# Kernel tuning notes

Hardware: AMD Instinct MI355X
Metric: run time of the kernel (lower is better)

The kernel has to match this reference:

```python
import jax, jax.numpy as jnp
import numpy as np


def setup_inputs() -> dict:
    key = jax.random.key(0)
    k1, k2, k3, k4, k5 = jax.random.split(key, 5)
    N, E, C_in, C_out = 100000, 1600000, 64, 64
    x = jax.random.normal(k1, (N, C_in), dtype=jnp.float32)
    edge_index = jax.random.randint(k2, (2, E), 0, N, dtype=jnp.int64)
    edge_weight = jax.random.uniform(k3, (E,), dtype=jnp.float32)
    # Xavier-uniform Linear weights [out, in], zero biases (matches reset_parameters)
    bound = float(np.sqrt(6.0 / (C_in + C_out)))
    W_self = jax.random.uniform(k4, (C_out, C_in), dtype=jnp.float32, minval=-bound, maxval=bound)
    W_neigh = jax.random.uniform(k5, (C_out, C_in), dtype=jnp.float32, minval=-bound, maxval=bound)
    b_self = jnp.zeros((C_out,), dtype=jnp.float32)
    b_neigh = jnp.zeros((C_out,), dtype=jnp.float32)
    return {"x": x, "edge_index": edge_index, "edge_weight": edge_weight,
            "W_self": W_self, "b_self": b_self, "W_neigh": W_neigh, "b_neigh": b_neigh,
            "num_nodes": N}


def reference(x, edge_index, edge_weight, W_self, b_self, W_neigh, b_neigh, num_nodes):
    row, col = edge_index[0], edge_index[1]
    # gather source features, weight, scatter-add to destinations: [E, C] -> [N, C]
    message = x[col] * edge_weight[:, None]
    neigh_agg = jax.ops.segment_sum(message, row, num_segments=num_nodes)
    # two linear projections (torch Linear: y = x @ W.T + b)
    return x @ W_self.T + b_self + neigh_agg @ W_neigh.T + b_neigh
```

## Files before the change

### kernel.cpp

```cpp
#include <hip/hip_runtime.h>
#include <hip/hip_bf16.h>


#define C 64
#define BKT 128
#define MAXB 800
#define BINT 6144
#define BTHR 1024
#define CAP 2560

typedef __attribute__((ext_vector_type(8))) short bf16x8;
typedef __attribute__((ext_vector_type(4))) float f32x4;

__device__ inline unsigned short f2bf(float f) {
    union { __hip_bfloat16 h; unsigned short u; } c;
    c.h = __float2bfloat16(f);
    return c.u;
}

__device__ inline float bfhi(unsigned short u) {
    return __int_as_float(((int)u) << 16);
}

__global__ __launch_bounds__(256) void prep_kernel(
        const int* __restrict__ ei, int* __restrict__ bhist, int E, int NBK,
        const float* __restrict__ x, unsigned short* __restrict__ xb, int n4) {
    __shared__ int lh[MAXB];
    const int t = threadIdx.x;
    for (int i = t; i < NBK; i += 256) lh[i] = 0;
    __syncthreads();
    const int gtid = blockIdx.x * 256 + t;
    const int gs = gridDim.x * 256;
    for (int e = gtid; e < E; e += gs)
        atomicAdd(&lh[ei[e] >> 7], 1);
    __syncthreads();
    for (int i = t; i < NBK; i += 256)
        if (lh[i]) atomicAdd(&bhist[i], lh[i]);
    const float4* x4 = (const float4*)x;
    ushort4* xb4 = (ushort4*)xb;
    for (int i = gtid; i < n4; i += gs) {
        float4 v = x4[i];
        ushort4 o;
        o.x = f2bf(v.x); o.y = f2bf(v.y); o.z = f2bf(v.z); o.w = f2bf(v.w);
        xb4[i] = o;
    }
}

__global__ __launch_bounds__(1024) void scan_kernel(
        const int* __restrict__ bhist, int* __restrict__ boffs,
        int* __restrict__ bcur, int NBK) {
    __shared__ int s[1024];
    const int t = threadIdx.x;
    s[t] = (t < NBK) ? bhist[t] : 0;
    __syncthreads();
    for (int off = 1; off < 1024; off <<= 1) {
        int v = 0;
        if (t >= off) v = s[t - off];
        __syncthreads();
        if (t >= off) s[t] += v;
        __syncthreads();
    }
    if (t < NBK) {
        int e = (t > 0) ? s[t - 1] : 0;
        boffs[t] = e;
        bcur[t] = e;
        if (t == NBK - 1) boffs[NBK] = s[t];
    }
}

__global__ __launch_bounds__(BTHR) void bin_kernel(
        const int* __restrict__ ei, const float* __restrict__ ew,
        int* __restrict__ bcur, const int* __restrict__ unused,
        int2* __restrict__ sorted, int E, int NBK) {
    __shared__ int2 stage[BINT];
    __shared__ unsigned short stageb[BINT];
    __shared__ int h[MAXB];
    __shared__ int cur[MAXB];
    __shared__ int adj[MAXB];
    __shared__ int wsum[16];

    const int t = threadIdx.x;
    const int lane = t & 63;
    const int wv = t >> 6;
    const int e0 = blockIdx.x * BINT;
    const int cnt = min(BINT, E - e0);

    for (int i = t; i < NBK; i += BTHR) h[i] = 0;
    __syncthreads();

#pragma unroll
    for (int k = 0; k < BINT / BTHR; ++k) {
        const int idx = t + k * BTHR;
        if (idx < cnt) atomicAdd(&h[ei[e0 + idx] >> 7], 1);
    }
    __syncthreads();

    const int val = (t < NBK) ? h[t] : 0;
    int v = val;
#pragma unroll
    for (int off = 1; off < 64; off <<= 1) {
        const int u = __shfl_up(v, off);
        if (lane >= off) v += u;
    }
    if (lane == 63) wsum[wv] = v;
    __syncthreads();
    if (t < 64) {
        int s = (lane < 16) ? wsum[lane] : 0;
#pragma unroll
        for (int off = 1; off < 16; off <<= 1) {
            const int u = __shfl_up(s, off);
            if (lane >= off) s += u;
        }
        if (lane < 16) wsum[lane] = s;
    }
    __syncthreads();
    if (t < NBK) {
        const int incl = v + ((wv > 0) ? wsum[wv - 1] : 0);
        const int excl = incl - val;
        cur[t] = excl;
        const int g = val ? atomicAdd(&bcur[t], val) : 0;
        adj[t] = g - excl;
    }
    __syncthreads();

#pragma unroll
    for (int k = 0; k < BINT / BTHR; ++k) {
        const int idx = t + k * BTHR;
        if (idx < cnt) {
            const int e = e0 + idx;
            const int d = ei[e];
            const int s = ei[E + e];
            const float w = ew[e];
            const int b = d >> 7;
            const int dl = d & 127;
            const int p = atomicAdd(&cur[b], 1);
            stage[p] = make_int2((dl << 17) | s, __float_as_int(w));
            stageb[p] = (unsigned short)b;
        }
    }
    __syncthreads();

    for (int i = t; i < cnt; i += BTHR) {
        const int b = stageb[i];
        sorted[adj[b] + i] = stage[i];
    }
}

__global__ __launch_bounds__(512) void agg_kernel(
        const ushort4* __restrict__ xb4,
        const int2* __restrict__ sorted,
        const int* __restrict__ boffs,
        float* __restrict__ agg, int N) {
    __shared__ int2 meta2[CAP];
    __shared__ int lcnt[BKT];
    __shared__ int lincl[BKT];
    __shared__ int lcur[BKT];

    const int t = threadIdx.x;
    const int b = blockIdx.x;
    const int node0 = b << 7;
    const int lane = t & 63;
    const int wv = t >> 6;
    const int q = lane >> 4;
    const int cq = lane & 15;

    const int beg = boffs[b];
    const int end = boffs[b + 1];

    int chunk = beg;
    do {
        const int cc = (end - chunk < CAP) ? (end - chunk) : CAP;

        for (int i = t; i < BKT; i += 512) lcnt[i] = 0;
        __syncthreads();

        for (int i = t; i < cc; i += 512)
            atomicAdd(&lcnt[sorted[chunk + i].x >> 17], 1);
        __syncthreads();

        if (t < BKT) lincl[t] = lcnt[t];
        __syncthreads();
        for (int off = 1; off < BKT; off <<= 1) {
            int v = 0;
            if (t < BKT && t >= off) v = lincl[t - off];
            __syncthreads();
            if (t < BKT && t >= off) lincl[t] += v;
            __syncthreads();
        }
        if (t < BKT) lcur[t] = lincl[t] - lcnt[t];
        __syncthreads();

        for (int i = t; i < cc; i += 512) {
            const int2 m = sorted[chunk + i];
            const int dl = m.x >> 17;
            const int p = atomicAdd(&lcur[dl], 1);
            meta2[p] = make_int2(m.x & 0x1FFFF, m.y);
        }
        __syncthreads();

        const bool first = (chunk == beg);
        for (int r = wv; r < BKT; r += 8) {
            const int s1 = lincl[r];
            const int s0 = s1 - lcnt[r];
            float a0 = 0.f, a1 = 0.f, a2 = 0.f, a3 = 0.f;
            int j = s0 + q;
            for (; j + 4 < s1; j += 8) {
                const int2 m0 = meta2[j];
                const int2 m1 = meta2[j + 4];
                const ushort4 u0 = xb4[(unsigned)m0.x * 16u + cq];
                const ushort4 u1 = xb4[(unsigned)m1.x * 16u + cq];
                const float w0 = __int_as_float(m0.y);
                const float w1 = __int_as_float(m1.y);
                a0 += w0 * bfhi(u0.x); a1 += w0 * bfhi(u0.y);
                a2 += w0 * bfhi(u0.z); a3 += w0 * bfhi(u0.w);
                a0 += w1 * bfhi(u1.x); a1 += w1 * bfhi(u1.y);
                a2 += w1 * bfhi(u1.z); a3 += w1 * bfhi(u1.w);
            }
            if (j < s1) {
                const int2 m0 = meta2[j];
                const ushort4 u0 = xb4[(unsigned)m0.x * 16u + cq];
                const float w0 = __int_as_float(m0.y);
                a0 += w0 * bfhi(u0.x); a1 += w0 * bfhi(u0.y);
                a2 += w0 * bfhi(u0.z); a3 += w0 * bfhi(u0.w);
            }
            a0 += __shfl_xor(a0, 16); a0 += __shfl_xor(a0, 32);
            a1 += __shfl_xor(a1, 16); a1 += __shfl_xor(a1, 32);
            a2 += __shfl_xor(a2, 16); a2 += __shfl_xor(a2, 32);
            a3 += __shfl_xor(a3, 16); a3 += __shfl_xor(a3, 32);
            const int node = node0 + r;
            if (q == 0 && node < N) {
                float4* dst = (float4*)(agg + (size_t)node * C + 4 * cq);
                if (first) {
                    *dst = make_float4(a0, a1, a2, a3);
                } else {
                    float4 o = *dst;
                    o.x += a0; o.y += a1; o.z += a2; o.w += a3;
                    *dst = o;
                }
            }
        }
        chunk += CAP;
        __syncthreads();
    } while (chunk < end);
}

__global__ __launch_bounds__(256) void scatter_kernel(
        const float* __restrict__ x, const int* __restrict__ ei,
        const float* __restrict__ ew, float* __restrict__ agg, int E) {
    const int lane = threadIdx.x & 63;
    const int wid = (blockIdx.x * blockDim.x + threadIdx.x) >> 6;
    const int nw = (gridDim.x * blockDim.x) >> 6;
    for (int base = wid * 64; base < E; base += nw * 64) {
        const int e = base + lane;
        int dst = 0, src = 0; float w = 0.f;
        if (e < E) { dst = ei[e]; src = ei[E + e]; w = ew[e]; }
        const int cnt = min(64, E - base);
        for (int j = 0; j < cnt; ++j) {
            const int d = __shfl(dst, j);
            const int s = __shfl(src, j);
            const float wj = __shfl(w, j);
            atomicAdd(&agg[d * C + lane], x[s * C + lane] * wj);
        }
    }
}

__device__ inline bf16x8 cvt8(const float* __restrict__ p) {
    f32x4 lo = *(const f32x4*)p;
    f32x4 hi = *(const f32x4*)(p + 4);
    union { bf16x8 v; __hip_bfloat16 e[8]; } u;
#pragma unroll
    for (int j = 0; j < 4; ++j) u.e[j] = __float2bfloat16(lo[j]);
#pragma unroll
    for (int j = 0; j < 4; ++j) u.e[4 + j] = __float2bfloat16(hi[j]);
    return u.v;
}

__global__ __launch_bounds__(256) void proj_kernel(
        const float* __restrict__ x, const float* __restrict__ agg,
        const float* __restrict__ Ws, const float* __restrict__ bs,
        const float* __restrict__ Wn, const float* __restrict__ bn,
        float* __restrict__ out, int N) {
    const int lane = threadIdx.x & 63;
    const int wid = (blockIdx.x * blockDim.x + threadIdx.x) >> 6;
    const int l15 = lane & 15;
    const int quad = lane >> 4;
    const int nTiles = N >> 4;
    if (wid >= nTiles) return;
    const int m0 = wid << 4;

    bf16x8 bsf[4][2], bnf[4][2];
#pragma unroll
    for (int tt = 0; tt < 4; ++tt) {
        const int o = tt * 16 + l15;
#pragma unroll
        for (int h = 0; h < 2; ++h) {
            bsf[tt][h] = cvt8(Ws + o * C + h * 32 + quad * 8);
            bnf[tt][h] = cvt8(Wn + o * C + h * 32 + quad * 8);
        }
    }

    const int m = m0 + l15;
    bf16x8 ax[2], ag[2];
#pragma unroll
    for (int h = 0; h < 2; ++h) {
        ax[h] = cvt8(x + m * C + h * 32 + quad * 8);
        ag[h] = cvt8(agg + m * C + h * 32 + quad * 8);
    }

#pragma unroll
    for (int tt = 0; tt < 4; ++tt) {
        f32x4 acc = {0.f, 0.f, 0.f, 0.f};
        acc = __builtin_amdgcn_mfma_f32_16x16x32_bf16(ax[0], bsf[tt][0], acc, 0, 0, 0);
        acc = __builtin_amdgcn_mfma_f32_16x16x32_bf16(ax[1], bsf[tt][1], acc, 0, 0, 0);
        acc = __builtin_amdgcn_mfma_f32_16x16x32_bf16(ag[0], bnf[tt][0], acc, 0, 0, 0);
        acc = __builtin_amdgcn_mfma_f32_16x16x32_bf16(ag[1], bnf[tt][1], acc, 0, 0, 0);
        const int o = tt * 16 + l15;
        const float bias = bs[o] + bn[o];
#pragma unroll
        for (int r = 0; r < 4; ++r)
            out[(m0 + quad * 4 + r) * C + o] = acc[r] + bias;
    }
}

extern "C" void kernel_launch(void* const* d_in, const int* in_sizes, int n_in,
                              void* d_out, int out_size, void* d_ws, size_t ws_size,
                              hipStream_t stream) {
    const float* x  = (const float*)d_in[0];
    const int*   ei = (const int*)d_in[1];
    const float* ew = (const float*)d_in[2];
    const float* Ws = (const float*)d_in[3];
    const float* bs = (const float*)d_in[4];
    const float* Wn = (const float*)d_in[5];
    const float* bn = (const float*)d_in[6];

    const int N = in_sizes[0] / C;
    const int E = in_sizes[2];
    const int NBK = (N + BKT - 1) / BKT;

    char* p = (char*)d_ws;
    float* agg = (float*)p;                 p += (size_t)N * C * sizeof(float);
    unsigned short* xb = (unsigned short*)p; p += (size_t)N * C * sizeof(short);
    int2* sorted = (int2*)p;                p += (size_t)E * sizeof(int2);
    int* bhist = (int*)p;                   p += (size_t)MAXB * sizeof(int);
    int* boffs = (int*)p;                   p += (size_t)(MAXB + 1) * sizeof(int);
    int* bcur = (int*)p;                    p += (size_t)MAXB * sizeof(int);
    const size_t needed = (size_t)(p - (char*)d_ws);

    const int nTiles = N / 16;
    const int projBlocks = (nTiles + 3) / 4;

    if (needed <= ws_size && N <= (1 << 17) && NBK <= MAXB) {
        const int n4 = N * C / 4;
        hipMemsetAsync(bhist, 0, (size_t)NBK * sizeof(int), stream);
        prep_kernel<<<1024, 256, 0, stream>>>(ei, bhist, E, NBK, x, xb, n4);
        scan_kernel<<<1, 1024, 0, stream>>>(bhist, boffs, bcur, NBK);
        bin_kernel<<<(E + BINT - 1) / BINT, BTHR, 0, stream>>>(ei, ew, bcur, bhist,
                                                               sorted, E, NBK);
        agg_kernel<<<NBK, 512, 0, stream>>>((const ushort4*)xb, sorted,
                                            boffs, agg, N);
    } else {
        hipMemsetAsync(agg, 0, (size_t)N * C * sizeof(float), stream);
        scatter_kernel<<<2048, 256, 0, stream>>>(x, ei, ew, agg, E);
    }

    proj_kernel<<<projBlocks, 256, 0, stream>>>(x, agg, Ws, bs, Wn, bn,
                                                (float*)d_out, N);
}
```

Baseline: 215.4 us.

## Widen agg gathers to 16B, write bf16 aggregate, add bf16-input projection

The aggregation kernel now loads 8 bf16 channels per lane with 16-byte loads, using 8 edge groups per wave instead of 4. It reduces the results with a transposing shuffle tree so every lane stores one channel. On the final chunk it writes the aggregate directly as bf16. A new projection kernel reads the bf16 x, the bf16 aggregate and the pre-converted bf16 weights, so the fp32 reads and in-kernel conversions disappear from the projection. The aim is fewer gather transactions and less projection traffic, at the cost of an extra bf16 buffer and more shuffle work.

```diff
diff --git a/kernel.cpp b/kernel.cpp
--- a/kernel.cpp
+++ b/kernel.cpp
@@ -18,13 +18,18 @@
     return c.u;
 }
 
-__device__ inline float bfhi(unsigned short u) {
-    return __int_as_float(((int)u) << 16);
+__device__ inline float bflo16(unsigned int u) {
+    return __int_as_float((int)(u << 16));
+}
+__device__ inline float bfhi16(unsigned int u) {
+    return __int_as_float((int)(u & 0xFFFF0000u));
 }
 
 __global__ __launch_bounds__(256) void prep_kernel(
         const int* __restrict__ ei, int* __restrict__ bhist, int E, int NBK,
-        const float* __restrict__ x, unsigned short* __restrict__ xb, int n4) {
+        const float* __restrict__ x, unsigned short* __restrict__ xb, int n4,
+        const float* __restrict__ Ws, const float* __restrict__ Wn,
+        unsigned short* __restrict__ Wsb, unsigned short* __restrict__ Wnb) {
     __shared__ int lh[MAXB];
     const int t = threadIdx.x;
     for (int i = t; i < NBK; i += 256) lh[i] = 0;
@@ -43,6 +48,15 @@
         ushort4 o;
         o.x = f2bf(v.x); o.y = f2bf(v.y); o.z = f2bf(v.z); o.w = f2bf(v.w);
         xb4[i] = o;
+    }
+    if (gtid < 1024) {
+        float4 v = ((const float4*)Ws)[gtid];
+        ushort4 o;
+        o.x = f2bf(v.x); o.y = f2bf(v.y); o.z = f2bf(v.z); o.w = f2bf(v.w);
+        ((ushort4*)Wsb)[gtid] = o;
+        v = ((const float4*)Wn)[gtid];
+        o.x = f2bf(v.x); o.y = f2bf(v.y); o.z = f2bf(v.z); o.w = f2bf(v.w);
+        ((ushort4*)Wnb)[gtid] = o;
     }
 }
 
@@ -147,10 +161,12 @@
 }
 
 __global__ __launch_bounds__(512) void agg_kernel(
-        const ushort4* __restrict__ xb4,
+        const unsigned short* __restrict__ xb,
         const int2* __restrict__ sorted,
         const int* __restrict__ boffs,
-        float* __restrict__ agg, int N) {
+        float* __restrict__ agg,
+        unsigned short* __restrict__ aggb,
+        int N) {
     __shared__ int2 meta2[CAP];
     __shared__ int lcnt[BKT];
     __shared__ int lincl[BKT];
@@ -161,8 +177,15 @@
     const int node0 = b << 7;
     const int lane = t & 63;
     const int wv = t >> 6;
-    const int q = lane >> 4;
-    const int cq = lane & 15;
+    const int oct = lane >> 3;
+    const int co = lane & 7;
+
+    const bool h1 = (lane & 8) != 0;
+    const bool h2 = (lane & 16) != 0;
+    const bool h3 = (lane & 32) != 0;
+    const int ch = co * 8 + (h1 ? 4 : 0) + (h2 ? 2 : 0) + (h3 ? 1 : 0);
+
+    const uint4* xb8 = (const uint4*)xb;
 
     const int beg = boffs[b];
     const int end = boffs[b + 1];
@@ -199,43 +222,63 @@
         __syncthreads();
 
         const bool first = (chunk == beg);
+        const bool last = (chunk + CAP >= end);
+
         for (int r = wv; r < BKT; r += 8) {
             const int s1 = lincl[r];
             const int s0 = s1 - lcnt[r];
             float a0 = 0.f, a1 = 0.f, a2 = 0.f, a3 = 0.f;
-            int j = s0 + q;
-            for (; j + 4 < s1; j += 8) {
+            float a4 = 0.f, a5 = 0.f, a6 = 0.f, a7 = 0.f;
+            int j = s0 + oct;
+            for (; j + 8 < s1; j += 16) {
                 const int2 m0 = meta2[j];
-                const int2 m1 = meta2[j + 4];
-                const ushort4 u0 = xb4[(unsigned)m0.x * 16u + cq];
-                const ushort4 u1 = xb4[(unsigned)m1.x * 16u + cq];
+                const int2 m1 = meta2[j + 8];
+                const uint4 u0 = xb8[(unsigned)m0.x * 8u + co];
+                const uint4 u1 = xb8[(unsigned)m1.x * 8u + co];
                 const float w0 = __int_as_float(m0.y);
                 const float w1 = __int_as_float(m1.y);
-                a0 += w0 * bfhi(u0.x); a1 += w0 * bfhi(u0.y);
-                a2 += w0 * bfhi(u0.z); a3 += w0 * bfhi(u0.w);
-                a0 += w1 * bfhi(u1.x); a1 += w1 * bfhi(u1.y);
-                a2 += w1 * bfhi(u1.z); a3 += w1 * bfhi(u1.w);
+                a0 += w0 * bflo16(u0.x); a1 += w0 * bfhi16(u0.x);
+                a2 += w0 * bflo16(u0.y); a3 += w0 * bfhi16(u0.y);
+                a4 += w0 * bflo16(u0.z); a5 += w0 * bfhi16(u0.z);
+                a6 += w0 * bflo16(u0.w); a7 += w0 * bfhi16(u0.w);
+                a0 += w1 * bflo16(u1.x); a1 += w1 * bfhi16(u1.x);
+                a2 += w1 * bflo16(u1.y); a3 += w1 * bfhi16(u1.y);
+                a4 += w1 * bflo16(u1.z); a5 += w1 * bfhi16(u1.z);
+                a6 += w1 * bflo16(u1.w); a7 += w1 * bfhi16(u1.w);
             }
             if (j < s1) {
                 const int2 m0 = meta2[j];
-                const ushort4 u0 = xb4[(unsigned)m0.x * 16u + cq];
+                const uint4 u0 = xb8[(unsigned)m0.x * 8u + co];
                 const float w0 = __int_as_float(m0.y);
-                a0 += w0 * bfhi(u0.x); a1 += w0 * bfhi(u0.y);
-                a2 += w0 * bfhi(u0.z); a3 += w0 * bfhi(u0.w);
+                a0 += w0 * bflo16(u0.x); a1 += w0 * bfhi16(u0.x);
+                a2 += w0 * bflo16(u0.y); a3 += w0 * bfhi16(u0.y);
+                a4 += w0 * bflo16(u0.z); a5 += w0 * bfhi16(u0.z);
+                a6 += w0 * bflo16(u0.w); a7 += w0 * bfhi16(u0.w);
             }
-            a0 += __shfl_xor(a0, 16); a0 += __shfl_xor(a0, 32);
-            a1 += __shfl_xor(a1, 16); a1 += __shfl_xor(a1, 32);
-            a2 += __shfl_xor(a2, 16); a2 += __shfl_xor(a2, 32);
-            a3 += __shfl_xor(a3, 16); a3 += __shfl_xor(a3, 32);
+            float r0 = __shfl_xor(h1 ? a0 : a4, 8);
+            float r1 = __shfl_xor(h1 ? a1 : a5, 8);
+            float r2 = __shfl_xor(h1 ? a2 : a6, 8);
+            float r3 = __shfl_xor(h1 ? a3 : a7, 8);
+            const float b0 = (h1 ? a4 : a0) + r0;
+            const float b1 = (h1 ? a5 : a1) + r1;
+            const float b2 = (h1 ? a6 : a2) + r2;
+            const float b3 = (h1 ? a7 : a3) + r3;
+            float r4 = __shfl_xor(h2 ? b0 : b2, 16);
+            float r5 = __shfl_xor(h2 ? b1 : b3, 16);
+            const float c0 = (h2 ? b2 : b0) + r4;
+            const float c1 = (h2 ? b3 : b1) + r5;
+            float r6 = __shfl_xor(h3 ? c0 : c1, 32);
+            float vfin = (h3 ? c1 : c0) + r6;
+
             const int node = node0 + r;
-            if (q == 0 && node < N) {
-                float4* dst = (float4*)(agg + (size_t)node * C + 4 * cq);
-                if (first) {
-                    *dst = make_float4(a0, a1, a2, a3);
+            if (node < N) {
+                const size_t off = (size_t)node * C + ch;
+                if (last) {
+                    if (!first) vfin += agg[off];
+                    aggb[off] = f2bf(vfin);
                 } else {
-                    float4 o = *dst;
-                    o.x += a0; o.y += a1; o.z += a2; o.w += a3;
-                    *dst = o;
+                    if (first) agg[off] = vfin;
+                    else       agg[off] += vfin;
                 }
             }
         }
@@ -322,6 +365,54 @@
     }
 }
 
+__global__ __launch_bounds__(256) void projb_kernel(
+        const unsigned short* __restrict__ xb,
+        const unsigned short* __restrict__ aggb,
+        const unsigned short* __restrict__ Wsb, const float* __restrict__ bs,
+        const unsigned short* __restrict__ Wnb, const float* __restrict__ bn,
+        float* __restrict__ out, int N) {
+    const int lane = threadIdx.x & 63;
+    const int wid = (blockIdx.x * blockDim.x + threadIdx.x) >> 6;
+    const int l15 = lane & 15;
+    const int quad = lane >> 4;
+    const int nTiles = N >> 4;
+    if (wid >= nTiles) return;
+    const int m0 = wid << 4;
+
+    bf16x8 bsf[4][2], bnf[4][2];
+#pragma unroll
+    for (int tt = 0; tt < 4; ++tt) {
+        const int o = tt * 16 + l15;
+#pragma unroll
+        for (int h = 0; h < 2; ++h) {
+            bsf[tt][h] = *(const bf16x8*)(Wsb + o * C + h * 32 + quad * 8);
+            bnf[tt][h] = *(const bf16x8*)(Wnb + o * C + h * 32 + quad * 8);
+        }
+    }
+
+    const int m = m0 + l15;
+    bf16x8 ax[2], ag[2];
+#pragma unroll
+    for (int h = 0; h < 2; ++h) {
+        ax[h] = *(const bf16x8*)(xb + (size_t)m * C + h * 32 + quad * 8);
+        ag[h] = *(const bf16x8*)(aggb + (size_t)m * C + h * 32 + quad * 8);
+    }
+
+#pragma unroll
+    for (int tt = 0; tt < 4; ++tt) {
+        f32x4 acc = {0.f, 0.f, 0.f, 0.f};
+        acc = __builtin_amdgcn_mfma_f32_16x16x32_bf16(ax[0], bsf[tt][0], acc, 0, 0, 0);
+        acc = __builtin_amdgcn_mfma_f32_16x16x32_bf16(ax[1], bsf[tt][1], acc, 0, 0, 0);
+        acc = __builtin_amdgcn_mfma_f32_16x16x32_bf16(ag[0], bnf[tt][0], acc, 0, 0, 0);
+        acc = __builtin_amdgcn_mfma_f32_16x16x32_bf16(ag[1], bnf[tt][1], acc, 0, 0, 0);
+        const int o = tt * 16 + l15;
+        const float bias = bs[o] + bn[o];
+#pragma unroll
+        for (int r = 0; r < 4; ++r)
+            out[(m0 + quad * 4 + r) * C + o] = acc[r] + bias;
+    }
+}
+
 extern "C" void kernel_launch(void* const* d_in, const int* in_sizes, int n_in,
                               void* d_out, int out_size, void* d_ws, size_t ws_size,
                               hipStream_t stream) {
@@ -338,12 +429,15 @@
     const int NBK = (N + BKT - 1) / BKT;
 
     char* p = (char*)d_ws;
-    float* agg = (float*)p;                 p += (size_t)N * C * sizeof(float);
-    unsigned short* xb = (unsigned short*)p; p += (size_t)N * C * sizeof(short);
-    int2* sorted = (int2*)p;                p += (size_t)E * sizeof(int2);
-    int* bhist = (int*)p;                   p += (size_t)MAXB * sizeof(int);
-    int* boffs = (int*)p;                   p += (size_t)(MAXB + 1) * sizeof(int);
-    int* bcur = (int*)p;                    p += (size_t)MAXB * sizeof(int);
+    float* agg = (float*)p;                  p += (size_t)N * C * sizeof(float);
+    unsigned short* xb = (unsigned short*)p;  p += (size_t)N * C * sizeof(short);
+    unsigned short* aggb = (unsigned short*)p; p += (size_t)N * C * sizeof(short);
+    int2* sorted = (int2*)p;                 p += (size_t)E * sizeof(int2);
+    unsigned short* Wsb = (unsigned short*)p; p += (size_t)C * C * sizeof(short);
+    unsigned short* Wnb = (unsigned short*)p; p += (size_t)C * C * sizeof(short);
+    int* bhist = (int*)p;                    p += (size_t)MAXB * sizeof(int);
+    int* boffs = (int*)p;                    p += (size_t)(MAXB + 1) * sizeof(int);
+    int* bcur = (int*)p;                     p += (size_t)MAXB * sizeof(int);
     const size_t needed = (size_t)(p - (char*)d_ws);
 
     const int nTiles = N / 16;
@@ -352,17 +446,18 @@
     if (needed <= ws_size && N <= (1 << 17) && NBK <= MAXB) {
         const int n4 = N * C / 4;
         hipMemsetAsync(bhist, 0, (size_t)NBK * sizeof(int), stream);
-        prep_kernel<<<1024, 256, 0, stream>>>(ei, bhist, E, NBK, x, xb, n4);
+        prep_kernel<<<1024, 256, 0, stream>>>(ei, bhist, E, NBK, x, xb, n4,
+                                              Ws, Wn, Wsb, Wnb);
         scan_kernel<<<1, 1024, 0, stream>>>(bhist, boffs, bcur, NBK);
         bin_kernel<<<(E + BINT - 1) / BINT, BTHR, 0, stream>>>(ei, ew, bcur, bhist,
                                                                sorted, E, NBK);
-        agg_kernel<<<NBK, 512, 0, stream>>>((const ushort4*)xb, sorted,
-                                            boffs, agg, N);
+        agg_kernel<<<NBK, 512, 0, stream>>>(xb, sorted, boffs, agg, aggb, N);
+        projb_kernel<<<projBlocks, 256, 0, stream>>>(xb, aggb, Wsb, bs, Wnb, bn,
+                                                     (float*)d_out, N);
     } else {
         hipMemsetAsync(agg, 0, (size_t)N * C * sizeof(float), stream);
         scatter_kernel<<<2048, 256, 0, stream>>>(x, ei, ew, agg, E);
-    }
-
-    proj_kernel<<<projBlocks, 256, 0, stream>>>(x, agg, Ws, bs, Wn, bn,
-                                                (float*)d_out, N);
-}
+        proj_kernel<<<projBlocks, 256, 0, stream>>>(x, agg, Ws, bs, Wn, bn,
+                                                    (float*)d_out, N);
+    }
+}
```

After: 194.5 us, median of 2. -9.7%, faster.
